# Optimization experiments

Measured on AMD Instinct MI355X. Metric: run time of the kernel, lower is better.

## Reference

```python
import jax, jax.numpy as jnp
import numpy as np

T, S, B = 512, 512, 8
D, H = 512, 8
HD = D // H
L = 8            # nlabels
F = 2048         # dim_feedforward
EPS = 1e-5


def _ln(x, s, b):
    m = x.mean(-1, keepdims=True)
    v = ((x - m) ** 2).mean(-1, keepdims=True)
    return (x - m) * jax.lax.rsqrt(v + EPS) * s + b


def setup_inputs() -> dict:
    key = jax.random.key(0)
    ks = jax.random.split(key, 20)
    p = lambda i, shape: jax.random.normal(ks[i], shape, jnp.float32) * 0.02
    z = lambda n: jnp.zeros((n,), jnp.float32)
    return {
        "tgt": jax.random.normal(ks[0], (T, B, D), jnp.float32),
        "edge_mask": jax.random.uniform(ks[1], (B, L, T, T), dtype=jnp.float32),
        "tgt_padding_mask": jnp.zeros((B, T, T), jnp.bool_),
        "memory": jax.random.normal(ks[2], (S, B, D), jnp.float32),
        # self-attn (GNN matrix relational attention)
        "sa_q_w": p(3, (D, D)), "sa_q_b": z(D),
        "sa_k_w": p(4, (D, D)), "sa_k_b": z(D),
        "sa_v_w": p(5, (D, D)), "sa_v_b": z(D),
        "sa_rel": p(6, (L, HD, HD)),
        "sa_out_w": p(7, (D, D)), "sa_out_b": z(D),
        # cross-attn (torch MultiheadAttention packed in_proj)
        "ca_in_w": p(8, (3 * D, D)), "ca_in_b": z(3 * D),
        "ca_out_w": p(9, (D, D)), "ca_out_b": z(D),
        # FFN
        "lin1_w": p(10, (F, D)), "lin1_b": z(F),
        "lin2_w": p(11, (D, F)), "lin2_b": z(D),
        # layernorms
        "ln1_s": jnp.ones((D,), jnp.float32), "ln1_b": z(D),
        "ln2_s": jnp.ones((D,), jnp.float32), "ln2_b": z(D),
        "ln3_s": jnp.ones((D,), jnp.float32), "ln3_b": z(D),
    }


def reference(tgt, edge_mask, tgt_padding_mask, memory,
              sa_q_w, sa_q_b, sa_k_w, sa_k_b, sa_v_w, sa_v_b, sa_rel,
              sa_out_w, sa_out_b, ca_in_w, ca_in_b, ca_out_w, ca_out_b,
              lin1_w, lin1_b, lin2_w, lin2_b,
              ln1_s, ln1_b, ln2_s, ln2_b, ln3_s, ln3_b):
    scale = 1.0 / np.sqrt(HD).astype(np.float32)

    # ---- edge-aware relational self-attention (dropout = eval/identity) ----
    x = tgt.transpose(1, 0, 2)                       # (B, T, D)
    def heads(y, n):                                 # (B, n, ., HD)
        return y.reshape(B, -1, H, HD).transpose(0, 2, 1, 3)
    q = heads(x @ sa_q_w.T + sa_q_b, T)
    k = heads(x @ sa_k_w.T + sa_k_b, T)
    v = heads(x @ sa_v_w.T + sa_v_b, T)

    scores = jnp.zeros((B, H, T, T), q.dtype)
    for l in range(L):                               # small fixed label set
        kl = jnp.einsum('bhtd,de->bhte', k, sa_rel[l])
        scores = scores + edge_mask[:, l][:, None] * jnp.einsum('bhid,bhjd->bhij', q, kl)
    scores = scores * scale
    scores = jnp.where(tgt_padding_mask[:, None], -1e9, scores)
    attn = jax.nn.softmax(scores, axis=-1)
    o = jnp.einsum('bhij,bhjd->bhid', attn, v).transpose(0, 2, 1, 3).reshape(B, T, D)
    tgt2 = (o @ sa_out_w.T + sa_out_b).transpose(1, 0, 2)   # (T, B, D)
    x1 = _ln(tgt + tgt2, ln1_s, ln1_b)

    # ---- standard cross-attention over encoder memory ----
    wq, wk, wv = ca_in_w[:D], ca_in_w[D:2 * D], ca_in_w[2 * D:]
    bq, bk, bv = ca_in_b[:D], ca_in_b[D:2 * D], ca_in_b[2 * D:]
    cq = heads((x1 @ wq.T + bq).transpose(1, 0, 2), T)       # (B,H,T,HD)
    ck = heads((memory @ wk.T + bk).transpose(1, 0, 2), S)   # (B,H,S,HD)
    cv = heads((memory @ wv.T + bv).transpose(1, 0, 2), S)
    cs = jnp.einsum('bhtd,bhsd->bhts', cq, ck) * scale
    ca = jax.nn.softmax(cs, axis=-1)
    co = jnp.einsum('bhts,bhsd->bhtd', ca, cv).transpose(0, 2, 1, 3).reshape(B, T, D)
    tgt2 = (co @ ca_out_w.T + ca_out_b).transpose(1, 0, 2)
    x2 = _ln(x1 + tgt2, ln2_s, ln2_b)

    # ---- FFN ----
    ffn = jax.nn.relu(x2 @ lin1_w.T + lin1_b) @ lin2_w.T + lin2_b
    return _ln(x2 + ffn, ln3_s, ln3_b)
```

## Files before the change

kernel.cpp:

```cpp
#include <hip/hip_runtime.h>

#define Tn 512
#define Sn 512
#define Bn 8
#define Dn 512
#define Hn 8
#define HDn 64
#define Ln 8
#define Fn 2048
#define SCALE 0.125f

typedef short short8 __attribute__((ext_vector_type(8)));
typedef float floatx4 __attribute__((ext_vector_type(4)));

__device__ __forceinline__ unsigned short f2b(float f) {
    unsigned int u = __float_as_uint(f);
    u += 0x7FFFu + ((u >> 16) & 1u);
    return (unsigned short)(u >> 16);
}

__global__ __launch_bounds__(256) void to_rows_bf16(const float* __restrict__ in,
                                                    unsigned short* __restrict__ out, int T_) {
    size_t n = (size_t)blockIdx.x * 256 + threadIdx.x;
    size_t total = (size_t)T_ * Bn * Dn;
    if (n >= total) return;
    int d = (int)(n & (Dn - 1));
    size_t rt = n >> 9;
    int t = (int)(rt % T_);
    int b = (int)(rt / T_);
    out[n] = f2b(in[((size_t)t * Bn + b) * Dn + d]);
}

__global__ __launch_bounds__(256) void conv_all(
    const float* __restrict__ qw, const float* __restrict__ kw, const float* __restrict__ vw,
    const float* __restrict__ sow, const float* __restrict__ ciw, const float* __restrict__ cow,
    const float* __restrict__ l1w, const float* __restrict__ l2w, const float* __restrict__ rel,
    const float* __restrict__ qbias, const float* __restrict__ kbias, const float* __restrict__ vbias,
    unsigned short* __restrict__ wall, float* __restrict__ bqkv) {
    const int Q = 1 << 18;
    const int total = 16 * Q + Ln * HDn * HDn;
    int i = blockIdx.x * 256 + threadIdx.x;
    if (i < total) {
        int seg = i >> 18, r = i & (Q - 1);
        float v;
        if (seg < 3)       v = (seg == 0 ? qw : (seg == 1 ? kw : vw))[r];
        else if (seg == 3) v = sow[r];
        else if (seg < 7)  v = ciw[(size_t)(seg - 4) * Q + r];
        else if (seg == 7) v = cow[r];
        else if (seg < 12) v = l1w[(size_t)(seg - 8) * Q + r];
        else if (seg < 16) v = l2w[(size_t)(seg - 12) * Q + r];
        else               v = rel[r];
        wall[i] = f2b(v);
    }
    int j = i - total;
    if (j >= 0 && j < 3 * Dn)
        bqkv[j] = (j < Dn ? qbias[j] : (j < 2 * Dn ? kbias[j - Dn] : vbias[j - 2 * Dn]));
}

__device__ __forceinline__ void c_scatter(
    floatx4 v, int gm, int gn, size_t coff, int ldc, float alpha, float bb,
    int mode, int relu, int Tp, void* Cv, void* Cv2, void* Cv3) {
    for (int r = 0; r < 4; ++r) {
        float val = v[r] * alpha + bb;
        if (relu) val = fmaxf(val, 0.0f);
        int m = gm + r;
        if (mode == 0) {
            ((float*)Cv)[coff + (size_t)m * ldc + gn] = val;
        } else if (mode == 1) {
            ((unsigned short*)Cv)[coff + (size_t)m * ldc + gn] = f2b(val);
        } else if (mode == 2) {
            int bq = m / Tp, t = m - bq * Tp;
            ((unsigned short*)Cv)[(((size_t)(bq * Hn + (gn >> 6)) * Tp + t) << 6) + (gn & 63)] = f2b(val);
        } else if (mode == 3) {
            int bq = m / Tp, t = m - bq * Tp;
            ((unsigned short*)Cv)[((size_t)(bq * Hn + (gn >> 6)) * 64 + (gn & 63)) * Tp + t] = f2b(val);
        } else if (mode == 4) {
            int sel = gn >> 9, g2 = gn & 511;
            int bq = m / Tp, t = m - bq * Tp;
            int hh = g2 >> 6, dd = g2 & 63;
            if (sel == 0)
                ((unsigned short*)Cv)[(((size_t)(bq * Hn + hh) * Tp + t) << 6) + dd] = f2b(val);
            else if (sel == 1)
                ((unsigned short*)Cv2)[(((size_t)(bq * Hn + hh) * Tp + t) << 6) + dd] = f2b(val);
            else
                ((unsigned short*)Cv3)[((size_t)(bq * Hn + hh) * 64 + dd) * Tp + t] = f2b(val);
        } else {
            int sel = gn >> 9, g2 = gn & 511;
            int bq = m / Tp, t = m - bq * Tp;
            int hh = g2 >> 6, dd = g2 & 63;
            if (sel == 0)
                ((unsigned short*)Cv)[(((size_t)(bq * Hn + hh) * Tp + t) << 6) + dd] = f2b(val);
            else
                ((unsigned short*)Cv2)[((size_t)(bq * Hn + hh) * 64 + dd) * Tp + t] = f2b(val);
        }
    }
}

__global__ __launch_bounds__(256) void gemm_bf16(
    const unsigned short* __restrict__ A, const unsigned short* __restrict__ W,
    const float* __restrict__ bias, void* __restrict__ Cv, void* __restrict__ Cv2,
    void* __restrict__ Cv3,
    int M, int N, int K, int lda, int ldw, int ldc,
    long sA1, long sA2, long sW1, long sW2, long sC1, long sC2, int zdiv,
    float alpha, int mode, int relu, int Tp) {
    int z = blockIdx.z;
    int z1 = z / zdiv, z2 = z - z1 * zdiv;
    const unsigned short* Ab = A + (size_t)z1 * sA1 + (size_t)z2 * sA2;
    const unsigned short* Wb = W + (size_t)z1 * sW1 + (size_t)z2 * sW2;
    size_t coff = (size_t)z1 * sC1 + (size_t)z2 * sC2;
    int tid = threadIdx.x;
    int lane = tid & 63, wave = tid >> 6;
    int wm = wave & 1, wn = wave >> 1;
    int l16 = lane & 15, quad = lane >> 4;
    int m0 = blockIdx.y * 64 + wm * 32;
    int n0 = blockIdx.x * 64 + wn * 32;

    floatx4 acc00 = {0,0,0,0}, acc01 = {0,0,0,0}, acc10 = {0,0,0,0}, acc11 = {0,0,0,0};
    const unsigned short* a0p = Ab + (size_t)(m0 + l16) * lda + quad * 8;
    const unsigned short* a1p = a0p + (size_t)16 * lda;
    const unsigned short* b0p = Wb + (size_t)(n0 + l16) * ldw + quad * 8;
    const unsigned short* b1p = b0p + (size_t)16 * ldw;

#pragma unroll 2
    for (int kk = 0; kk < K; kk += 32) {
        short8 a0 = *(const short8*)(a0p + kk);
        short8 a1 = *(const short8*)(a1p + kk);
        short8 b0 = *(const short8*)(b0p + kk);
        short8 b1 = *(const short8*)(b1p + kk);
        acc00 = __builtin_amdgcn_mfma_f32_16x16x32_bf16(a0, b0, acc00, 0, 0, 0);
        acc01 = __builtin_amdgcn_mfma_f32_16x16x32_bf16(a0, b1, acc01, 0, 0, 0);
        acc10 = __builtin_amdgcn_mfma_f32_16x16x32_bf16(a1, b0, acc10, 0, 0, 0);
        acc11 = __builtin_amdgcn_mfma_f32_16x16x32_bf16(a1, b1, acc11, 0, 0, 0);
    }
    floatx4 accs[2][2] = {{acc00, acc01}, {acc10, acc11}};
    for (int mt = 0; mt < 2; ++mt)
        for (int nt = 0; nt < 2; ++nt) {
            int gn = n0 + nt * 16 + l16;
            float bb = bias ? bias[gn] : 0.0f;
            c_scatter(accs[mt][nt], m0 + mt * 16 + quad * 4, gn, coff, ldc,
                      alpha, bb, mode, relu, Tp, Cv, Cv2, Cv3);
        }
}

template <int MT, int NT>
__global__ __launch_bounds__(256) void gemmT_bf16(
    const unsigned short* __restrict__ A, const unsigned short* __restrict__ W,
    const float* __restrict__ bias, void* __restrict__ Cv, void* __restrict__ Cv2,
    void* __restrict__ Cv3,
    int K, int lda, int ldw, int ldc,
    float alpha, int mode, int relu, int Tp) {
    int tid = threadIdx.x;
    int lane = tid & 63, wave = tid >> 6;
    int wm = wave & 1, wn = wave >> 1;
    int l16 = lane & 15, quad = lane >> 4;
    int m0 = blockIdx.y * (MT * 32) + wm * (MT * 16);
    int n0 = blockIdx.x * (NT * 32) + wn * (NT * 16);

    floatx4 acc[MT][NT] = {};
    const unsigned short* ap = A + (size_t)(m0 + l16) * lda + quad * 8;
    const unsigned short* bp = W + (size_t)(n0 + l16) * ldw + quad * 8;

    for (int kk = 0; kk < K; kk += 32) {
        short8 a[MT], b[NT];
#pragma unroll
        for (int mt = 0; mt < MT; ++mt)
            a[mt] = *(const short8*)(ap + (size_t)mt * 16 * lda + kk);
#pragma unroll
        for (int nt = 0; nt < NT; ++nt)
            b[nt] = *(const short8*)(bp + (size_t)nt * 16 * ldw + kk);
#pragma unroll
        for (int mt = 0; mt < MT; ++mt)
#pragma unroll
            for (int nt = 0; nt < NT; ++nt)
                acc[mt][nt] = __builtin_amdgcn_mfma_f32_16x16x32_bf16(a[mt], b[nt], acc[mt][nt], 0, 0, 0);
    }
    for (int mt = 0; mt < MT; ++mt)
        for (int nt = 0; nt < NT; ++nt) {
            int gn = n0 + nt * 16 + l16;
            float bb = bias ? bias[gn] : 0.0f;
            c_scatter(acc[mt][nt], m0 + mt * 16 + quad * 4, gn, 0, ldc,
                      alpha, bb, mode, relu, Tp, Cv, Cv2, Cv3);
        }
}

template <int NL, bool EM>
__global__ __launch_bounds__(256) void relsoft(
    const unsigned short* __restrict__ uR,
    const unsigned short* __restrict__ kB,
    const float* __restrict__ em,
    const unsigned char* __restrict__ pad,
    unsigned short* __restrict__ P) {
    int id = blockIdx.x;
    int c = id & 7, h = (id >> 3) & 7, g = id >> 6;
    int u = g * 8 + c;
    int b = u >> 5, it = u & 31;
    int bh = b * Hn + h;
    int wave = threadIdx.x >> 6, lane = threadIdx.x & 63;
    int l16 = lane & 15, quad = lane >> 4;
    int i = it * 16 + l16;

    const int JC = Tn / 64;

    const unsigned short* kp0 = kB + (size_t)bh * Tn * HDn + (size_t)l16 * HDn + quad * 8;
    short8 kf[JC][2];
#pragma unroll
    for (int jc = 0; jc < JC; ++jc) {
        const unsigned short* kp = kp0 + (size_t)(wave * JC + jc) * 16 * HDn;
        kf[jc][0] = *(const short8*)(kp);
        kf[jc][1] = *(const short8*)(kp + 32);
    }

    const unsigned short* ub = uR + (size_t)bh * NL * Tn * HDn + (size_t)i * HDn + quad * 8;
    const float* emB = EM ? (em + ((size_t)b * NL * Tn + i) * Tn) : nullptr;

    floatx4 sacc[JC] = {};
#pragma clang loop unroll(disable)
    for (int l = 0; l < NL; ++l) {
        short8 u0 = *(const short8*)(ub + (size_t)l * Tn * HDn);
        short8 u1 = *(const short8*)(ub + (size_t)l * Tn * HDn + 32);
#pragma unroll
        for (int jc = 0; jc < JC; ++jc) {
            int jt = wave * JC + jc;
            floatx4 gacc = {0, 0, 0, 0};
            gacc = __builtin_amdgcn_mfma_f32_16x16x32_bf16(kf[jc][0], u0, gacc, 0, 0, 0);
            gacc = __builtin_amdgcn_mfma_f32_16x16x32_bf16(kf[jc][1], u1, gacc, 0, 0, 0);
            if (EM) {
                floatx4 e4 = *(const floatx4*)(emB + (size_t)l * Tn * Tn + jt * 16 + quad * 4);
                sacc[jc] += e4 * gacc;
            } else {
                sacc[jc] = gacc;
            }
        }
    }

    float mx = -3.0e38f;
    for (int jc = 0; jc < JC; ++jc) {
        int jt = wave * JC + jc;
        floatx4 v = sacc[jc] * SCALE;
        if (EM) {
            unsigned int pu = *(const unsigned int*)(pad + ((size_t)b * Tn + i) * Tn + jt * 16 + quad * 4);
            if (pu) {
                if (pu & 0x000000FFu) v[0] = -1.0e9f;
                if (pu & 0x0000FF00u) v[1] = -1.0e9f;
                if (pu & 0x00FF0000u) v[2] = -1.0e9f;
                if (pu & 0xFF000000u) v[3] = -1.0e9f;
            }
        }
        sacc[jc] = v;
        mx = fmaxf(mx, fmaxf(fmaxf(v[0], v[1]), fmaxf(v[2], v[3])));
    }
    mx = fmaxf(mx, __shfl_xor(mx, 16, 64));
    mx = fmaxf(mx, __shfl_xor(mx, 32, 64));

    __shared__ float redm[4][16];
    __shared__ float reds[4][16];
    if (quad == 0) redm[wave][l16] = mx;
    __syncthreads();
    mx = fmaxf(fmaxf(redm[0][l16], redm[1][l16]), fmaxf(redm[2][l16], redm[3][l16]));

    float sum = 0.0f;
    for (int jc = 0; jc < JC; ++jc) {
        floatx4 v = sacc[jc];
        v[0] = __expf(v[0] - mx); v[1] = __expf(v[1] - mx);
        v[2] = __expf(v[2] - mx); v[3] = __expf(v[3] - mx);
        sacc[jc] = v;
        sum += v[0] + v[1] + v[2] + v[3];
    }
    sum += __shfl_xor(sum, 16, 64);
    sum += __shfl_xor(sum, 32, 64);
    if (quad == 0) reds[wave][l16] = sum;
    __syncthreads();
    sum = (reds[0][l16] + reds[1][l16]) + (reds[2][l16] + reds[3][l16]);
    float inv = 1.0f / sum;

    unsigned short* prow = P + (size_t)bh * Tn * Tn + (size_t)i * Tn;
    for (int jc = 0; jc < JC; ++jc) {
        int jt = wave * JC + jc;
        floatx4 v = sacc[jc];
        ushort4 o;
        o.x = f2b(v[0] * inv); o.y = f2b(v[1] * inv);
        o.z = f2b(v[2] * inv); o.w = f2b(v[3] * inv);
        *(ushort4*)(prow + jt * 16 + quad * 4) = o;
    }
}

__global__ __launch_bounds__(256) void ln_kernel(
    const float* __restrict__ a, int a_trans, const float* __restrict__ b2,
    const float* __restrict__ s, const float* __restrict__ bb,
    float* __restrict__ outF, int out_trans, unsigned short* __restrict__ outB) {
    int row = blockIdx.x;
    int b = row >> 9, t = row & (Tn - 1);
    int tid = threadIdx.x;
    size_t ia = a_trans ? ((size_t)(t * Bn + b)) * Dn : (size_t)row * Dn;
    size_t ir = (size_t)row * Dn;
    float x0 = a[ia + tid];
    float x1 = a[ia + tid + 256];
    if (b2) { x0 += b2[ir + tid]; x1 += b2[ir + tid + 256]; }
    float s1 = x0 + x1, s2 = x0 * x0 + x1 * x1;
    for (int off = 32; off; off >>= 1) {
        s1 += __shfl_xor(s1, off, 64);
        s2 += __shfl_xor(s2, off, 64);
    }
    __shared__ float red[2][4];
    int wave = tid >> 6, lane = tid & 63;
    if (lane == 0) { red[0][wave] = s1; red[1][wave] = s2; }
    __syncthreads();
    float ts1 = red[0][0] + red[0][1] + red[0][2] + red[0][3];
    float ts2 = red[1][0] + red[1][1] + red[1][2] + red[1][3];
    float mean = ts1 * (1.0f / Dn);
    float var = ts2 * (1.0f / Dn) - mean * mean;
    float rs = rsqrtf(var + 1e-5f);
    float y0 = (x0 - mean) * rs * s[tid] + bb[tid];
    float y1 = (x1 - mean) * rs * s[tid + 256] + bb[tid + 256];
    size_t io = out_trans ? ((size_t)(t * Bn + b)) * Dn : ir;
    if (outF) { outF[io + tid] = y0; outF[io + tid + 256] = y1; }
    if (outB) { outB[ir + tid] = f2b(y0); outB[ir + tid + 256] = f2b(y1); }
}

extern "C" void kernel_launch(void* const* d_in, const int* in_sizes, int n_in,
                              void* d_out, int out_size, void* d_ws, size_t ws_size,
                              hipStream_t stream) {
    const float* tgt      = (const float*)d_in[0];
    const float* em       = (const float*)d_in[1];
    const unsigned char* pad = (const unsigned char*)d_in[2];
    const float* memr     = (const float*)d_in[3];
    const float* sa_q_w   = (const float*)d_in[4];
    const float* sa_q_b   = (const float*)d_in[5];
    const float* sa_k_w   = (const float*)d_in[6];
    const float* sa_k_b   = (const float*)d_in[7];
    const float* sa_v_w   = (const float*)d_in[8];
    const float* sa_v_b   = (const float*)d_in[9];
    const float* sa_rel   = (const float*)d_in[10];
    const float* sa_out_w = (const float*)d_in[11];
    const float* sa_out_b = (const float*)d_in[12];
    const float* ca_in_w  = (const float*)d_in[13];
    const float* ca_in_b  = (const float*)d_in[14];
    const float* ca_out_w = (const float*)d_in[15];
    const float* ca_out_b = (const float*)d_in[16];
    const float* lin1_w   = (const float*)d_in[17];
    const float* lin1_b   = (const float*)d_in[18];
    const float* lin2_w   = (const float*)d_in[19];
    const float* lin2_b   = (const float*)d_in[20];
    const float* ln1_s    = (const float*)d_in[21];
    const float* ln1_b    = (const float*)d_in[22];
    const float* ln2_s    = (const float*)d_in[23];
    const float* ln2_b    = (const float*)d_in[24];
    const float* ln3_s    = (const float*)d_in[25];
    const float* ln3_b    = (const float*)d_in[26];

    const size_t BT = (size_t)Bn * Tn;
    const size_t Q  = 1 << 18;

    char* ws = (char*)d_ws;
    size_t off = 0;
    auto alloc = [&](size_t bytes) -> char* {
        char* p = ws + off;
        off += (bytes + 255) & ~(size_t)255;
        return p;
    };
    unsigned short* xb   = (unsigned short*)alloc(BT * Dn * 2);
    unsigned short* mb   = (unsigned short*)alloc(BT * Dn * 2);
    unsigned short* wall = (unsigned short*)alloc((16 * Q + Ln * HDn * HDn) * 2);
    float*          bqkv = (float*)alloc(3 * Dn * 4);
    unsigned short* qb   = (unsigned short*)alloc(BT * Dn * 2);
    unsigned short* kb   = (unsigned short*)alloc(BT * Dn * 2);
    unsigned short* vtb  = (unsigned short*)alloc(BT * Dn * 2);
    unsigned short* ur   = (unsigned short*)alloc((size_t)Bn * Hn * Ln * Tn * HDn * 2);
    unsigned short* pb   = (unsigned short*)alloc((size_t)Bn * Hn * Tn * Tn * 2);
    unsigned short* ob   = (unsigned short*)alloc(BT * Dn * 2);
    float*          t2f  = (float*)alloc(BT * Dn * 4);
    float*          x1f  = (float*)alloc(BT * Dn * 4);
    unsigned short* x1b  = (unsigned short*)alloc(BT * Dn * 2);
    float*          x2f  = (float*)alloc(BT * Dn * 4);
    unsigned short* x2b  = (unsigned short*)alloc(BT * Dn * 2);
    unsigned short* hid  = (unsigned short*)alloc(BT * Fn * 2);
    (void)ws_size; (void)in_sizes; (void)n_in; (void)out_size;

    unsigned short* wqkv = wall;
    unsigned short* wsao = wall + 3 * Q;
    unsigned short* wcain = wall + 4 * Q;
    unsigned short* wcao = wall + 7 * Q;
    unsigned short* wlin1 = wall + 8 * Q;
    unsigned short* wlin2 = wall + 12 * Q;
    unsigned short* wrel = wall + 16 * Q;

    auto gemm = [&](const unsigned short* A, const unsigned short* W, const float* bias,
                    void* C, void* C2, void* C3, int M, int N, int K, int lda, int ldw, int ldc,
                    long sA1, long sA2, long sW1, long sW2, long sC1, long sC2,
                    int zdiv, int batches, float alpha, int mode, int relu, int Tp) {
        dim3 g(N / 64, M / 64, batches);
        gemm_bf16<<<g, 256, 0, stream>>>(A, W, bias, C, C2, C3, M, N, K, lda, ldw, ldc,
                                         sA1, sA2, sW1, sW2, sC1, sC2, zdiv,
                                         alpha, mode, relu, Tp);
    };
    auto gemmBig = [&](const unsigned short* A, const unsigned short* W, const float* bias,
                       void* C, void* C2, void* C3, int M, int N, int K,
                       int lda, int ldw, int ldc, float alpha, int mode, int relu, int Tp) {
        dim3 g(N / 128, M / 128, 1);
        gemmT_bf16<4, 4><<<g, 256, 0, stream>>>(A, W, bias, C, C2, C3, K, lda, ldw, ldc,
                                                alpha, mode, relu, Tp);
    };
    auto gemmMed = [&](const unsigned short* A, const unsigned short* W, const float* bias,
                       void* C, void* C2, void* C3, int M, int N, int K,
                       int lda, int ldw, int ldc, float alpha, int mode, int relu, int Tp) {
        dim3 g(N / 64, M / 128, 1);
        gemmT_bf16<4, 2><<<g, 256, 0, stream>>>(A, W, bias, C, C2, C3, K, lda, ldw, ldc,
                                                alpha, mode, relu, Tp);
    };

    to_rows_bf16<<<dim3((BT * Dn + 255) / 256), 256, 0, stream>>>(tgt, xb, Tn);
    to_rows_bf16<<<dim3((BT * Dn + 255) / 256), 256, 0, stream>>>(memr, mb, Sn);
    conv_all<<<dim3((16 * Q + Ln * HDn * HDn + 3 * Dn + 255) / 256), 256, 0, stream>>>(
        sa_q_w, sa_k_w, sa_v_w, sa_out_w, ca_in_w, ca_out_w, lin1_w, lin2_w, sa_rel,
        sa_q_b, sa_k_b, sa_v_b, wall, bqkv);

    gemmBig(xb, wqkv, bqkv, qb, kb, vtb, (int)BT, 3 * Dn, Dn, Dn, Dn, 0, 1.0f, 4, 0, Tn);
    gemm(qb, wrel, nullptr, ur, nullptr, nullptr, Tn, HDn, HDn, HDn, HDn, HDn,
         (long)Tn * HDn, 0, 0, (long)HDn * HDn, (long)Ln * Tn * HDn, (long)Tn * HDn,
         Ln, Bn * Hn * Ln, 1.0f, 1, 0, 0);
    relsoft<Ln, true><<<dim3(2048), 256, 0, stream>>>(ur, kb, em, pad, pb);
    gemm(pb, vtb, nullptr, ob, nullptr, nullptr, Tn, HDn, Tn, Tn, Tn, Dn,
         (long)Hn * Tn * Tn, (long)Tn * Tn, (long)Hn * HDn * Tn, (long)HDn * Tn,
         (long)Tn * Dn, 64, Hn, Bn * Hn, 1.0f, 1, 0, 0);
    gemmMed(ob, wsao, sa_out_b, t2f, nullptr, nullptr, (int)BT, Dn, Dn, Dn, Dn, Dn,
            1.0f, 0, 0, 0);
    ln_kernel<<<dim3((int)BT), 256, 0, stream>>>(tgt, 1, t2f, ln1_s, ln1_b, x1f, 0, x1b);

    gemmMed(x1b, wcain, ca_in_b, qb, nullptr, nullptr, (int)BT, Dn, Dn, Dn, Dn, 0,
            1.0f, 2, 0, Tn);
    gemmBig(mb, wcain + (size_t)Dn * Dn, ca_in_b + Dn, kb, vtb, nullptr, (int)BT, 2 * Dn, Dn,
            Dn, Dn, 0, 1.0f, 5, 0, Sn);
    relsoft<1, false><<<dim3(2048), 256, 0, stream>>>(qb, kb, nullptr, nullptr, pb);
    gemm(pb, vtb, nullptr, ob, nullptr, nullptr, Tn, HDn, Sn, Sn, Sn, Dn,
         (long)Hn * Tn * Sn, (long)Tn * Sn, (long)Hn * HDn * Sn, (long)HDn * Sn,
         (long)Tn * Dn, 64, Hn, Bn * Hn, 1.0f, 1, 0, 0);
    gemmMed(ob, wcao, ca_out_b, t2f, nullptr, nullptr, (int)BT, Dn, Dn, Dn, Dn, Dn,
            1.0f, 0, 0, 0);
    ln_kernel<<<dim3((int)BT), 256, 0, stream>>>(x1f, 0, t2f, ln2_s, ln2_b, x2f, 0, x2b);

    gemmBig(x2b, wlin1, lin1_b, hid, nullptr, nullptr, (int)BT, Fn, Dn, Dn, Dn, Fn,
            1.0f, 1, 1, 0);
    gemmMed(hid, wlin2, lin2_b, t2f, nullptr, nullptr, (int)BT, Dn, Fn, Fn, Fn, Dn,
            1.0f, 0, 0, 0);
    ln_kernel<<<dim3((int)BT), 256, 0, stream>>>(x2f, 0, t2f, ln3_s, ln3_b, (float*)d_out, 1, nullptr);
}
```

Baseline: 664.5 us.

## Double-buffer edge-mask tiles into LDS via async global_load_lds in relsoft

```diff
diff --git a/kernel.cpp b/kernel.cpp
--- a/kernel.cpp
+++ b/kernel.cpp
@@ -201,6 +201,31 @@
 
     const int JC = Tn / 64;
 
+    __shared__ float emS[EM ? 2 * 4 * 512 * 4 : 4];
+    __shared__ float redm[4][16];
+    __shared__ float reds[4][16];
+
+    const float* emRow = nullptr;
+    if constexpr (EM)
+        emRow = em + ((size_t)b * NL * Tn + (size_t)it * 16) * Tn;
+
+    auto stage = [&](int l, int buf) {
+        const float* rowb = emRow + (size_t)l * Tn * Tn;
+        float* wb = emS + (size_t)(buf * 4 + wave) * 512 * 4;
+#pragma unroll
+        for (int k = 0; k < 8; ++k) {
+            int s = k * 64 + lane;
+            int ii = s >> 5, c32 = s & 31;
+            const float* gp = rowb + (size_t)ii * Tn + ((wave * 32) + (c32 ^ (ii & 7))) * 4;
+            __builtin_amdgcn_global_load_lds(
+                (const __attribute__((address_space(1))) void*)gp,
+                (__attribute__((address_space(3))) void*)(wb + k * 64 * 4),
+                16, 0, 0);
+        }
+    };
+
+    if constexpr (EM) stage(0, 0);
+
     const unsigned short* kp0 = kB + (size_t)bh * Tn * HDn + (size_t)l16 * HDn + quad * 8;
     short8 kf[JC][2];
 #pragma unroll
@@ -211,26 +236,39 @@
     }
 
     const unsigned short* ub = uR + (size_t)bh * NL * Tn * HDn + (size_t)i * HDn + quad * 8;
-    const float* emB = EM ? (em + ((size_t)b * NL * Tn + i) * Tn) : nullptr;
+    short8 u0 = *(const short8*)(ub);
+    short8 u1 = *(const short8*)(ub + 32);
 
     floatx4 sacc[JC] = {};
 #pragma clang loop unroll(disable)
     for (int l = 0; l < NL; ++l) {
-        short8 u0 = *(const short8*)(ub + (size_t)l * Tn * HDn);
-        short8 u1 = *(const short8*)(ub + (size_t)l * Tn * HDn + 32);
+        int buf = l & 1;
+        if constexpr (EM) {
+            asm volatile("s_waitcnt vmcnt(0)" ::: "memory");
+        }
+        if (l + 1 < NL) {
+            if constexpr (EM) stage(l + 1, buf ^ 1);
+        }
+        short8 nu0, nu1;
+        if (l + 1 < NL) {
+            nu0 = *(const short8*)(ub + (size_t)(l + 1) * Tn * HDn);
+            nu1 = *(const short8*)(ub + (size_t)(l + 1) * Tn * HDn + 32);
+        }
+        const float* rb = emS + (size_t)(buf * 4 + wave) * 512 * 4;
 #pragma unroll
         for (int jc = 0; jc < JC; ++jc) {
-            int jt = wave * JC + jc;
             floatx4 gacc = {0, 0, 0, 0};
             gacc = __builtin_amdgcn_mfma_f32_16x16x32_bf16(kf[jc][0], u0, gacc, 0, 0, 0);
             gacc = __builtin_amdgcn_mfma_f32_16x16x32_bf16(kf[jc][1], u1, gacc, 0, 0, 0);
             if (EM) {
-                floatx4 e4 = *(const floatx4*)(emB + (size_t)l * Tn * Tn + jt * 16 + quad * 4);
+                int q = l16 * 32 + ((jc * 4 + quad) ^ (l16 & 7));
+                floatx4 e4 = *(const floatx4*)(rb + (size_t)q * 4);
                 sacc[jc] += e4 * gacc;
             } else {
                 sacc[jc] = gacc;
             }
         }
+        if (l + 1 < NL) { u0 = nu0; u1 = nu1; }
     }
 
     float mx = -3.0e38f;
@@ -252,8 +290,6 @@
     mx = fmaxf(mx, __shfl_xor(mx, 16, 64));
     mx = fmaxf(mx, __shfl_xor(mx, 32, 64));
 
-    __shared__ float redm[4][16];
-    __shared__ float reds[4][16];
     if (quad == 0) redm[wave][l16] = mx;
     __syncthreads();
     mx = fmaxf(fmaxf(redm[0][l16], redm[1][l16]), fmaxf(redm[2][l16], redm[3][l16]));
```

New measurement: 628.7 us. -5.4%, faster.

## Restructure edge-aware softmax to share edge_mask tiles across heads via LDS

Applied to the files above, without the earlier changes.

```diff
diff --git a/kernel.cpp b/kernel.cpp
--- a/kernel.cpp
+++ b/kernel.cpp
@@ -183,12 +183,159 @@
         }
 }
 
-template <int NL, bool EM>
-__global__ __launch_bounds__(256) void relsoft(
+__global__ __launch_bounds__(512, 2) void relsoft_em(
     const unsigned short* __restrict__ uR,
     const unsigned short* __restrict__ kB,
     const float* __restrict__ em,
     const unsigned char* __restrict__ pad,
+    unsigned short* __restrict__ P) {
+    int b = blockIdx.x >> 5, it = blockIdx.x & 31;
+    int tid = threadIdx.x;
+    int wave = tid >> 6, lane = tid & 63;
+    int l16 = lane & 15, quad = lane >> 4;
+    int i = it * 16 + l16;
+
+    __shared__ float emS[2 * 8192];
+    __shared__ float redm[2][8][16];
+    __shared__ float reds[2][8][16];
+
+    auto stage = [&](int step) {
+        int l = step & 7, buf = step & 1;
+        const float* rowb = em + (((size_t)b * Ln + l) * Tn + (size_t)it * 16) * Tn;
+#pragma unroll
+        for (int k = 0; k < 4; ++k) {
+            int s = k * 512 + wave * 64 + lane;
+            int is = s >> 7, gs = s & 127;
+            int colg = (gs & 120) | ((gs & 7) ^ (is & 7));
+            const float* gp = rowb + (size_t)is * Tn + colg * 4;
+            __builtin_amdgcn_global_load_lds(
+                (const __attribute__((address_space(1))) void*)gp,
+                (__attribute__((address_space(3))) void*)(emS + (size_t)buf * 8192 +
+                                                         (size_t)(k * 512 + wave * 64) * 4),
+                16, 0, 0);
+        }
+    };
+
+    unsigned int puf[4];
+#pragma unroll
+    for (int jc = 0; jc < 4; ++jc)
+        puf[jc] = *(const unsigned int*)(pad + ((size_t)b * Tn + i) * Tn +
+                                         wave * 64 + jc * 16 + quad * 4);
+
+    stage(0);
+
+#pragma clang loop unroll(disable)
+    for (int hp = 0; hp < 4; ++hp) {
+        int h0 = hp * 2;
+        short8 kf[2][4][2];
+#pragma unroll
+        for (int hh = 0; hh < 2; ++hh)
+#pragma unroll
+            for (int jc = 0; jc < 4; ++jc) {
+                const unsigned short* kp = kB + (((size_t)(b * Hn + h0 + hh) * Tn) +
+                                                wave * 64 + jc * 16 + l16) * HDn + quad * 8;
+                kf[hh][jc][0] = *(const short8*)(kp);
+                kf[hh][jc][1] = *(const short8*)(kp + 32);
+            }
+        floatx4 sacc[2][4] = {};
+
+#pragma clang loop unroll(disable)
+        for (int l = 0; l < Ln; ++l) {
+            int step = hp * 8 + l;
+            int buf = l & 1;
+            asm volatile("s_waitcnt vmcnt(0)");
+            __builtin_amdgcn_sched_barrier(0);
+            __syncthreads();
+            if (step + 1 < 32) stage(step + 1);
+
+            const float* rb = emS + (size_t)buf * 8192;
+            floatx4 emr[4];
+#pragma unroll
+            for (int jc = 0; jc < 4; ++jc) {
+                int gg = wave * 16 + jc * 4 + quad;
+                int gsw = (gg & 120) | ((gg & 7) ^ (l16 & 7));
+                emr[jc] = *(const floatx4*)(rb + (size_t)(l16 * 128 + gsw) * 4);
+            }
+            const unsigned short* up = uR + ((((size_t)(b * Hn + h0) * Ln + l) * Tn) + i) * HDn + quad * 8;
+            short8 u0a = *(const short8*)(up);
+            short8 u0b = *(const short8*)(up + 32);
+            short8 u1a = *(const short8*)(up + (size_t)Ln * Tn * HDn);
+            short8 u1b = *(const short8*)(up + (size_t)Ln * Tn * HDn + 32);
+#pragma unroll
+            for (int jc = 0; jc < 4; ++jc) {
+                floatx4 g0 = {0, 0, 0, 0};
+                g0 = __builtin_amdgcn_mfma_f32_16x16x32_bf16(kf[0][jc][0], u0a, g0, 0, 0, 0);
+                g0 = __builtin_amdgcn_mfma_f32_16x16x32_bf16(kf[0][jc][1], u0b, g0, 0, 0, 0);
+                sacc[0][jc] += emr[jc] * g0;
+                floatx4 g1 = {0, 0, 0, 0};
+                g1 = __builtin_amdgcn_mfma_f32_16x16x32_bf16(kf[1][jc][0], u1a, g1, 0, 0, 0);
+                g1 = __builtin_amdgcn_mfma_f32_16x16x32_bf16(kf[1][jc][1], u1b, g1, 0, 0, 0);
+                sacc[1][jc] += emr[jc] * g1;
+            }
+        }
+
+#pragma unroll
+        for (int hh = 0; hh < 2; ++hh) {
+            float mx = -3.0e38f;
+#pragma unroll
+            for (int jc = 0; jc < 4; ++jc) {
+                floatx4 v = sacc[hh][jc] * SCALE;
+                unsigned int pu = puf[jc];
+                if (pu) {
+                    if (pu & 0x000000FFu) v[0] = -1.0e9f;
+                    if (pu & 0x0000FF00u) v[1] = -1.0e9f;
+                    if (pu & 0x00FF0000u) v[2] = -1.0e9f;
+                    if (pu & 0xFF000000u) v[3] = -1.0e9f;
+                }
+                sacc[hh][jc] = v;
+                mx = fmaxf(mx, fmaxf(fmaxf(v[0], v[1]), fmaxf(v[2], v[3])));
+            }
+            mx = fmaxf(mx, __shfl_xor(mx, 16, 64));
+            mx = fmaxf(mx, __shfl_xor(mx, 32, 64));
+            if (quad == 0) redm[hh][wave][l16] = mx;
+        }
+        __syncthreads();
+#pragma unroll
+        for (int hh = 0; hh < 2; ++hh) {
+            float m = redm[hh][0][l16];
+#pragma unroll
+            for (int w = 1; w < 8; ++w) m = fmaxf(m, redm[hh][w][l16]);
+            float sum = 0.0f;
+#pragma unroll
+            for (int jc = 0; jc < 4; ++jc) {
+                floatx4 v = sacc[hh][jc];
+                v[0] = __expf(v[0] - m); v[1] = __expf(v[1] - m);
+                v[2] = __expf(v[2] - m); v[3] = __expf(v[3] - m);
+                sacc[hh][jc] = v;
+                sum += v[0] + v[1] + v[2] + v[3];
+            }
+            sum += __shfl_xor(sum, 16, 64);
+            sum += __shfl_xor(sum, 32, 64);
+            if (quad == 0) reds[hh][wave][l16] = sum;
+        }
+        __syncthreads();
+#pragma unroll
+        for (int hh = 0; hh < 2; ++hh) {
+            float sum = 0.0f;
+#pragma unroll
+            for (int w = 0; w < 8; ++w) sum += reds[hh][w][l16];
+            float inv = 1.0f / sum;
+            unsigned short* prow = P + ((size_t)(b * Hn + h0 + hh) * Tn + i) * Tn;
+#pragma unroll
+            for (int jc = 0; jc < 4; ++jc) {
+                floatx4 v = sacc[hh][jc];
+                ushort4 o;
+                o.x = f2b(v[0] * inv); o.y = f2b(v[1] * inv);
+                o.z = f2b(v[2] * inv); o.w = f2b(v[3] * inv);
+                *(ushort4*)(prow + wave * 64 + jc * 16 + quad * 4) = o;
+            }
+        }
+    }
+}
+
+__global__ __launch_bounds__(256) void relsoft_nc(
+    const unsigned short* __restrict__ qB,
+    const unsigned short* __restrict__ kB,
     unsigned short* __restrict__ P) {
     int id = blockIdx.x;
     int c = id & 7, h = (id >> 3) & 7, g = id >> 6;
@@ -198,10 +345,12 @@
     int wave = threadIdx.x >> 6, lane = threadIdx.x & 63;
     int l16 = lane & 15, quad = lane >> 4;
     int i = it * 16 + l16;
-
-    const int JC = Tn / 64;
-
-    const unsigned short* kp0 = kB + (size_t)bh * Tn * HDn + (size_t)l16 * HDn + quad * 8;
+    const int JC = Sn / 64;
+
+    __shared__ float redm[4][16];
+    __shared__ float reds[4][16];
+
+    const unsigned short* kp0 = kB + (size_t)bh * Sn * HDn + (size_t)l16 * HDn + quad * 8;
     short8 kf[JC][2];
 #pragma unroll
     for (int jc = 0; jc < JC; ++jc) {
@@ -209,56 +358,29 @@
         kf[jc][0] = *(const short8*)(kp);
         kf[jc][1] = *(const short8*)(kp + 32);
     }
-
-    const unsigned short* ub = uR + (size_t)bh * NL * Tn * HDn + (size_t)i * HDn + quad * 8;
-    const float* emB = EM ? (em + ((size_t)b * NL * Tn + i) * Tn) : nullptr;
-
-    floatx4 sacc[JC] = {};
-#pragma clang loop unroll(disable)
-    for (int l = 0; l < NL; ++l) {
-        short8 u0 = *(const short8*)(ub + (size_t)l * Tn * HDn);
-        short8 u1 = *(const short8*)(ub + (size_t)l * Tn * HDn + 32);
-#pragma unroll
-        for (int jc = 0; jc < JC; ++jc) {
-            int jt = wave * JC + jc;
-            floatx4 gacc = {0, 0, 0, 0};
-            gacc = __builtin_amdgcn_mfma_f32_16x16x32_bf16(kf[jc][0], u0, gacc, 0, 0, 0);
-            gacc = __builtin_amdgcn_mfma_f32_16x16x32_bf16(kf[jc][1], u1, gacc, 0, 0, 0);
-            if (EM) {
-                floatx4 e4 = *(const floatx4*)(emB + (size_t)l * Tn * Tn + jt * 16 + quad * 4);
-                sacc[jc] += e4 * gacc;
-            } else {
-                sacc[jc] = gacc;
-            }
-        }
-    }
-
+    const unsigned short* ub = qB + (size_t)bh * Tn * HDn + (size_t)i * HDn + quad * 8;
+    short8 u0 = *(const short8*)(ub);
+    short8 u1 = *(const short8*)(ub + 32);
+
+    floatx4 sacc[JC];
     float mx = -3.0e38f;
+#pragma unroll
     for (int jc = 0; jc < JC; ++jc) {
-        int jt = wave * JC + jc;
-        floatx4 v = sacc[jc] * SCALE;
-        if (EM) {
-            unsigned int pu = *(const unsigned int*)(pad + ((size_t)b * Tn + i) * Tn + jt * 16 + quad * 4);
-            if (pu) {
-                if (pu & 0x000000FFu) v[0] = -1.0e9f;
-                if (pu & 0x0000FF00u) v[1] = -1.0e9f;
-                if (pu & 0x00FF0000u) v[2] = -1.0e9f;
-                if (pu & 0xFF000000u) v[3] = -1.0e9f;
-            }
-        }
+        floatx4 gacc = {0, 0, 0, 0};
+        gacc = __builtin_amdgcn_mfma_f32_16x16x32_bf16(kf[jc][0], u0, gacc, 0, 0, 0);
+        gacc = __builtin_amdgcn_mfma_f32_16x16x32_bf16(kf[jc][1], u1, gacc, 0, 0, 0);
+        floatx4 v = gacc * SCALE;
         sacc[jc] = v;
         mx = fmaxf(mx, fmaxf(fmaxf(v[0], v[1]), fmaxf(v[2], v[3])));
     }
     mx = fmaxf(mx, __shfl_xor(mx, 16, 64));
     mx = fmaxf(mx, __shfl_xor(mx, 32, 64));
-
-    __shared__ float redm[4][16];
-    __shared__ float reds[4][16];
     if (quad == 0) redm[wave][l16] = mx;
     __syncthreads();
     mx = fmaxf(fmaxf(redm[0][l16], redm[1][l16]), fmaxf(redm[2][l16], redm[3][l16]));
 
     float sum = 0.0f;
+#pragma unroll
     for (int jc = 0; jc < JC; ++jc) {
         floatx4 v = sacc[jc];
         v[0] = __expf(v[0] - mx); v[1] = __expf(v[1] - mx);
@@ -273,7 +395,8 @@
     sum = (reds[0][l16] + reds[1][l16]) + (reds[2][l16] + reds[3][l16]);
     float inv = 1.0f / sum;
 
-    unsigned short* prow = P + (size_t)bh * Tn * Tn + (size_t)i * Tn;
+    unsigned short* prow = P + (size_t)bh * Tn * Sn + (size_t)i * Sn;
+#pragma unroll
     for (int jc = 0; jc < JC; ++jc) {
         int jt = wave * JC + jc;
         floatx4 v = sacc[jc];
@@ -418,7 +541,7 @@
     gemm(qb, wrel, nullptr, ur, nullptr, nullptr, Tn, HDn, HDn, HDn, HDn, HDn,
          (long)Tn * HDn, 0, 0, (long)HDn * HDn, (long)Ln * Tn * HDn, (long)Tn * HDn,
          Ln, Bn * Hn * Ln, 1.0f, 1, 0, 0);
-    relsoft<Ln, true><<<dim3(2048), 256, 0, stream>>>(ur, kb, em, pad, pb);
+    relsoft_em<<<dim3(256), 512, 0, stream>>>(ur, kb, em, pad, pb);
     gemm(pb, vtb, nullptr, ob, nullptr, nullptr, Tn, HDn, Tn, Tn, Tn, Dn,
          (long)Hn * Tn * Tn, (long)Tn * Tn, (long)Hn * HDn * Tn, (long)HDn * Tn,
          (long)Tn * Dn, 64, Hn, Bn * Hn, 1.0f, 1, 0, 0);
@@ -430,7 +553,7 @@
             1.0f, 2, 0, Tn);
     gemmBig(mb, wcain + (size_t)Dn * Dn, ca_in_b + Dn, kb, vtb, nullptr, (int)BT, 2 * Dn, Dn,
             Dn, Dn, 0, 1.0f, 5, 0, Sn);
-    relsoft<1, false><<<dim3(2048), 256, 0, stream>>>(qb, kb, nullptr, nullptr, pb);
+    relsoft_nc<<<dim3(2048), 256, 0, stream>>>(qb, kb, pb);
     gemm(pb, vtb, nullptr, ob, nullptr, nullptr, Tn, HDn, Sn, Sn, Sn, Dn,
          (long)Hn * Tn * Sn, (long)Tn * Sn, (long)Hn * HDn * Sn, (long)HDn * Sn,
          (long)Tn * Dn, 64, Hn, Bn * Hn, 1.0f, 1, 0, 0);
```

Result: faster. 641.7 us (-3.4%).
